# Kernel optimization log

Hardware: AMD Instinct MI355X
Metric: run time of the kernel (lower is better)

The kernel has to match this reference:

```python
import jax, jax.numpy as jnp
import numpy as np
from jax import lax

B, C, T, K, L, G = 4, 256, 2048, 7, 2, 32


def _conv1d(x, w, b, pad=0, groups=1):
    # x: [B,C,T], w: [O, C//groups, kw]
    y = lax.conv_general_dilated(x, w, window_strides=(1,), padding=[(pad, pad)],
                                 dimension_numbers=("NCH", "OIH", "NCH"),
                                 feature_group_count=groups)
    return y + b[None, :, None]


def _conv2d(x, w, b, pad=(0, 0), groups=1):
    # x: [B,C,H,W], w: [O, C//groups, kh, kw]
    y = lax.conv_general_dilated(x, w, window_strides=(1, 1),
                                 padding=[(pad[0], pad[0]), (pad[1], pad[1])],
                                 dimension_numbers=("NCHW", "OIHW", "NCHW"),
                                 feature_group_count=groups)
    return y + b[None, :, None, None]


def _knn_dis(x, k):
    # x: [B,C,T] -> neighbor indices [B,T,k] by (negative) squared euclidean distance
    xx = jnp.sum(x * x, axis=1)                       # [B,T]
    inner = jnp.einsum("bcm,bcn->bmn", x, x)          # [B,T,T]
    pd = -xx[:, :, None] + 2.0 * inner - xx[:, None, :]  # -||x_m - x_n||^2
    _, idx = lax.top_k(pd, k)                          # nearest = largest of -dist^2
    return idx


def _graph_feature(x, idx):
    # x: [B,C,T], idx: [B,T,K] -> style=1 feature [B,2C,T,K] = cat(neighbor, center)
    xt = jnp.transpose(x, (0, 2, 1))                   # [B,T,C]
    bidx = jnp.arange(x.shape[0])[:, None, None]
    nb = xt[bidx, idx]                                 # [B,T,K,C] gather
    ctr = jnp.broadcast_to(xt[:, :, None, :], nb.shape)
    feat = jnp.concatenate([nb, ctr], axis=-1)         # [B,T,K,2C]
    return jnp.transpose(feat, (0, 3, 1, 2))           # [B,2C,T,K]


def setup_inputs() -> dict:
    key = jax.random.key(0)
    ks = jax.random.split(key, 9)
    s = 0.05
    return {
        "x": jax.random.normal(ks[0], (B, C, T), jnp.float32),
        "tw1": jax.random.normal(ks[1], (L, C, C, 1), jnp.float32) * s,
        "tb1": jax.random.normal(ks[2], (L, C), jnp.float32) * s,
        "tw2": jax.random.normal(ks[3], (L, C, C // G, 5), jnp.float32) * s,
        "tb2": jax.random.normal(ks[4], (L, C), jnp.float32) * s,
        "dw1": jax.random.normal(ks[5], (L, C, 2 * C, 1, 1), jnp.float32) * s,
        "db1": jax.random.normal(ks[6], (L, C), jnp.float32) * s,
        "dw2": jax.random.normal(ks[7], (L, C, C // G, 5, 5), jnp.float32) * s,
        "db2": jax.random.normal(ks[8], (L, C), jnp.float32) * s,
    }


def reference(x, tw1, tb1, tw2, tb2, dw1, db1, dw2, db2):
    for i in range(L):
        identity = x
        # temporal branch: 1x1 conv -> GELU -> grouped conv1d k=5 (pad=2)
        h = jax.nn.gelu(_conv1d(x, tw1[i], tb1[i]), approximate=False)
        tout = _conv1d(h, tw2[i], tb2[i], pad=2, groups=G)            # [B,C,T]
        # dynamic graph branch: euclidean knn -> gather -> DConv2D -> max over k
        idx = _knn_dis(x, K)                                           # [B,T,K]
        feat = _graph_feature(x, idx)                                  # [B,2C,T,K]
        g = jax.nn.gelu(_conv2d(feat, dw1[i], db1[i]), approximate=False)
        g = _conv2d(g, dw2[i], db2[i], pad=(2, 2), groups=G)          # [B,C,T,K]
        dout = jnp.max(g, axis=-1)                                     # [B,C,T]
        x = tout + dout + identity
    return x
```

## Files before the change

kernel.cpp:

```cpp
#include <hip/hip_runtime.h>
#include <math.h>

#define Bq 4
#define Cc 256
#define Tt 2048
#define Kk 7
#define NTOP 10
#define CG 8
#define Ll 2
#define NO 768

typedef __attribute__((ext_vector_type(8))) short short8;
typedef __attribute__((ext_vector_type(4))) float floatx4;
typedef __attribute__((ext_vector_type(2))) float floatx2;

__device__ __forceinline__ float gelu_f(float v) {
  return 0.5f * v * (1.0f + erff(v * 0.70710678118654752440f));
}

__device__ __forceinline__ float erf_fast(float x) {
  float ax = fabsf(x);
  float t = __builtin_amdgcn_rcpf(fmaf(0.3275911f, ax, 1.0f));
  float y = t * (0.254829592f + t * (-0.284496736f + t * (1.421413741f +
            t * (-1.453152027f + t * 1.061405429f))));
  float r = 1.0f - y * __expf(-ax * ax);
  return copysignf(r, x);
}
__device__ __forceinline__ float gelu_fast(float v) {
  return 0.5f * v * (1.0f + erf_fast(v * 0.70710678118654752440f));
}

__global__ void transpose_x(const float* __restrict__ x, float* __restrict__ xT,
                            unsigned short* __restrict__ xh,
                            unsigned short* __restrict__ xl) {
  __shared__ float tile[32][33];
  int b = blockIdx.z;
  int t0 = blockIdx.x * 32, c0 = blockIdx.y * 32;
  int tx = threadIdx.x, ty = threadIdx.y;
  const float* xb = x + (size_t)b * Cc * Tt;
  for (int r = ty; r < 32; r += 8)
    tile[r][tx] = xb[(size_t)(c0 + r) * Tt + t0 + tx];
  __syncthreads();
  size_t base = (size_t)b * Tt * Cc;
  for (int r = ty; r < 32; r += 8) {
    float v = tile[tx][r];
    size_t o = base + (size_t)(t0 + r) * Cc + c0 + tx;
    xT[o] = v;
    unsigned int u = __float_as_uint(v);
    unsigned short h = (unsigned short)((u + 0x7fffu + ((u >> 16) & 1u)) >> 16);
    float f = v - __uint_as_float((unsigned int)h << 16);
    unsigned int ul = __float_as_uint(f);
    xh[o] = h;
    xl[o] = (unsigned short)((ul + 0x7fffu + ((ul >> 16) & 1u)) >> 16);
  }
}

__global__ __launch_bounds__(512) void sqnorm_xt(
    const float* __restrict__ xT, float* __restrict__ xx) {
  int b = blockIdx.y;
  int t = blockIdx.x * 8 + (threadIdx.x >> 6);
  int lane = threadIdx.x & 63;
  const float* row = xT + ((size_t)b * Tt + t) * Cc;
  float4 v = *(const float4*)(row + lane * 4);
  float acc = v.x * v.x + v.y * v.y + v.z * v.z + v.w * v.w;
#pragma unroll
  for (int off = 1; off < 64; off <<= 1) acc += __shfl_xor(acc, off);
  if (lane == 0) xx[(size_t)b * Tt + t] = acc;
}

__global__ __launch_bounds__(256) void pw_conv8_all(
    const float* __restrict__ x, const float* __restrict__ tw1,
    const float* __restrict__ tb1, const float* __restrict__ dw1,
    const float* __restrict__ db1, float* __restrict__ hb,
    float* __restrict__ cb, float* __restrict__ nt) {
  int tid = threadIdx.x;
  int wv = tid >> 6, lane = tid & 63;
  int t = blockIdx.x * 1024 + wv * 256 + lane * 4;
  int oy = blockIdx.y;
  int b = blockIdx.z;
  int range = oy >> 5;
  int o0 = (oy & 31) * 8;
  const float* W; int wstride, woff; const float* bias; int dg;
  if (range == 0)      { W = tw1; wstride = Cc;     woff = 0;  bias = tb1;     dg = 1; }
  else if (range == 1) { W = dw1; wstride = 2 * Cc; woff = Cc; bias = db1;     dg = 0; }
  else                 { W = dw1; wstride = 2 * Cc; woff = 0;  bias = nullptr; dg = 0; }
  const float* xp = x + (size_t)b * Cc * Tt + t;
  const float* wp = W + (size_t)o0 * wstride + woff;
  float acc[8][4];
#pragma unroll
  for (int j = 0; j < 8; ++j) {
    float bv = bias ? bias[o0 + j] : 0.f;
#pragma unroll
    for (int e = 0; e < 4; ++e) acc[j][e] = bv;
  }
  for (int c = 0; c < Cc; c += 4) {
    float4 xv0 = *(const float4*)(xp + (size_t)c * Tt);
    float4 xv1 = *(const float4*)(xp + (size_t)(c + 1) * Tt);
    float4 xv2 = *(const float4*)(xp + (size_t)(c + 2) * Tt);
    float4 xv3 = *(const float4*)(xp + (size_t)(c + 3) * Tt);
    float x0[4] = {xv0.x, xv0.y, xv0.z, xv0.w};
    float x1[4] = {xv1.x, xv1.y, xv1.z, xv1.w};
    float x2[4] = {xv2.x, xv2.y, xv2.z, xv2.w};
    float x3[4] = {xv3.x, xv3.y, xv3.z, xv3.w};
#pragma unroll
    for (int j = 0; j < 8; ++j) {
      const float* wr = wp + (size_t)j * wstride + c;
      float w0 = wr[0], w1 = wr[1], w2 = wr[2], w3 = wr[3];
#pragma unroll
      for (int e = 0; e < 4; ++e) {
        float a = acc[j][e];
        a = fmaf(w0, x0[e], a);
        a = fmaf(w1, x1[e], a);
        a = fmaf(w2, x2[e], a);
        a = fmaf(w3, x3[e], a);
        acc[j][e] = a;
      }
    }
  }
  if (range == 2) {
    float* nb0 = nt + ((size_t)b * Tt + t) * Cc + o0;
#pragma unroll
    for (int e = 0; e < 4; ++e) {
      float4 r0, r1;
      r0.x = acc[0][e]; r0.y = acc[1][e]; r0.z = acc[2][e]; r0.w = acc[3][e];
      r1.x = acc[4][e]; r1.y = acc[5][e]; r1.z = acc[6][e]; r1.w = acc[7][e];
      *(float4*)&nb0[(size_t)e * Cc] = r0;
      *(float4*)&nb0[(size_t)e * Cc + 4] = r1;
    }
  } else {
    float* dst = (range == 0) ? hb : cb;
#pragma unroll
    for (int j = 0; j < 8; ++j) {
      float4 r;
      float* rp = (float*)&r;
#pragma unroll
      for (int e = 0; e < 4; ++e) {
        float v = acc[j][e];
        if (dg) v = gelu_f(v);
        rp[e] = v;
      }
      *(float4*)&dst[((size_t)b * Cc + o0 + j) * Tt + t] = r;
    }
  }
}

__global__ __launch_bounds__(256) void wsplit(
    const float* __restrict__ tw1, const float* __restrict__ dw1,
    unsigned short* __restrict__ wh, unsigned short* __restrict__ wl) {
  int o = blockIdx.x;
  int c = threadIdx.x;
  float v;
  if (o < 256) v = tw1[(size_t)o * Cc + c];
  else if (o < 512) v = dw1[(size_t)(o - 256) * (2 * Cc) + Cc + c];
  else v = dw1[(size_t)(o - 512) * (2 * Cc) + c];
  unsigned int u = __float_as_uint(v);
  unsigned short h = (unsigned short)((u + 0x7fffu + ((u >> 16) & 1u)) >> 16);
  float f = v - __uint_as_float((unsigned int)h << 16);
  unsigned int ul = __float_as_uint(f);
  wh[(size_t)o * Cc + c] = h;
  wl[(size_t)o * Cc + c] = (unsigned short)((ul + 0x7fffu + ((ul >> 16) & 1u)) >> 16);
}

__global__ __launch_bounds__(256) void pw_gemm(
    const unsigned short* __restrict__ wh, const unsigned short* __restrict__ wl,
    const unsigned short* __restrict__ xh, const unsigned short* __restrict__ xl,
    const float* __restrict__ tb1, const float* __restrict__ db1,
    float* __restrict__ hb, float* __restrict__ cb, float* __restrict__ nt) {
  __shared__ __align__(16) unsigned short Ah[128][40], Al[128][40];
  __shared__ __align__(16) unsigned short Bh[128][40], Bl[128][40];
  int mt = blockIdx.x;
  int b = mt >> 4;
  int t0 = (mt & 15) * 128;
  int o0 = blockIdx.y * 128;
  int tid = threadIdx.x;
  int w = tid >> 6, lane = tid & 63, quad = lane >> 4, l15 = lane & 15;
  int wm = (w >> 1) * 64, wn = (w & 1) * 64;
  floatx4 acc[4][4];
#pragma unroll
  for (int i = 0; i < 4; ++i)
#pragma unroll
    for (int j = 0; j < 4; ++j) acc[i][j] = (floatx4){0.f, 0.f, 0.f, 0.f};

  const unsigned short* xhb = xh + ((size_t)b * Tt + t0) * Cc;
  const unsigned short* xlb = xl + ((size_t)b * Tt + t0) * Cc;
  int sr = tid >> 1;
  int sq = (tid & 1) * 2;
  for (int kc = 0; kc < Cc; kc += 32) {
    __syncthreads();
    {
      const unsigned short* am = wh + (size_t)(o0 + sr) * Cc + kc + sq * 8;
      *(uint4*)&Ah[sr][sq * 8] = *(const uint4*)am;
      *(uint4*)&Ah[sr][sq * 8 + 8] = *(const uint4*)(am + 8);
      const unsigned short* al = wl + (size_t)(o0 + sr) * Cc + kc + sq * 8;
      *(uint4*)&Al[sr][sq * 8] = *(const uint4*)al;
      *(uint4*)&Al[sr][sq * 8 + 8] = *(const uint4*)(al + 8);
      const unsigned short* bm = xhb + (size_t)sr * Cc + kc + sq * 8;
      *(uint4*)&Bh[sr][sq * 8] = *(const uint4*)bm;
      *(uint4*)&Bh[sr][sq * 8 + 8] = *(const uint4*)(bm + 8);
      const unsigned short* bl = xlb + (size_t)sr * Cc + kc + sq * 8;
      *(uint4*)&Bl[sr][sq * 8] = *(const uint4*)bl;
      *(uint4*)&Bl[sr][sq * 8 + 8] = *(const uint4*)(bl + 8);
    }
    __syncthreads();
    int ka = quad * 8;
    short8 a_h[4], a_l[4], b_h[4], b_l[4];
#pragma unroll
    for (int f = 0; f < 4; ++f) {
      a_h[f] = *(const short8*)&Ah[wm + f * 16 + l15][ka];
      a_l[f] = *(const short8*)&Al[wm + f * 16 + l15][ka];
      b_h[f] = *(const short8*)&Bh[wn + f * 16 + l15][ka];
      b_l[f] = *(const short8*)&Bl[wn + f * 16 + l15][ka];
    }
#pragma unroll
    for (int fm = 0; fm < 4; ++fm)
#pragma unroll
      for (int fn = 0; fn < 4; ++fn) {
        acc[fm][fn] = __builtin_amdgcn_mfma_f32_16x16x32_bf16(a_h[fm], b_h[fn], acc[fm][fn], 0, 0, 0);
        acc[fm][fn] = __builtin_amdgcn_mfma_f32_16x16x32_bf16(a_h[fm], b_l[fn], acc[fm][fn], 0, 0, 0);
        acc[fm][fn] = __builtin_amdgcn_mfma_f32_16x16x32_bf16(a_l[fm], b_h[fn], acc[fm][fn], 0, 0, 0);
      }
  }
  int range = o0 >> 8;
  int ol0 = o0 & 255;
  if (range == 2) {
#pragma unroll
    for (int fm = 0; fm < 4; ++fm) {
      int o = ol0 + wm + fm * 16 + quad * 4;
#pragma unroll
      for (int r = 0; r < 4; ++r) {
#pragma unroll
        for (int fn = 0; fn < 4; ++fn) {
          int t = wn + fn * 16 + l15;
          nt[((size_t)b * Tt + t0 + t) * Cc + o + r] = acc[fm][fn][r];
        }
      }
    }
  } else {
    float* dst = (range == 0) ? hb : cb;
    const float* bias = (range == 0) ? tb1 : db1;
#pragma unroll
    for (int fm = 0; fm < 4; ++fm) {
      int o = ol0 + wm + fm * 16 + quad * 4;
#pragma unroll
      for (int r = 0; r < 4; ++r) {
        float bv = bias[o + r];
        size_t rowoff = ((size_t)b * Cc + o + r) * Tt + t0;
#pragma unroll
        for (int fn = 0; fn < 4; ++fn) {
          int t = wn + fn * 16 + l15;
          float v = acc[fm][fn][r] + bv;
          if (range == 0) v = gelu_f(v);
          dst[rowoff + t] = v;
        }
      }
    }
  }
}

__global__ __launch_bounds__(256) void score_gemm(
    const unsigned short* __restrict__ xh, const unsigned short* __restrict__ xl,
    const float* __restrict__ xx, float* __restrict__ S, int bbase) {
  __shared__ __align__(16) unsigned short Ah[128][40], Al[128][40];
  __shared__ __align__(16) unsigned short Bh[128][40], Bl[128][40];
  int lb = blockIdx.z;
  int b = bbase + lb;
  int m0 = blockIdx.y * 128, n0 = blockIdx.x * 128;
  int tid = threadIdx.x;
  int w = tid >> 6, lane = tid & 63, quad = lane >> 4, l15 = lane & 15;
  int wm = (w >> 1) * 64, wn = (w & 1) * 64;
  const unsigned short* xhb = xh + (size_t)b * Tt * Cc;
  const unsigned short* xlb = xl + (size_t)b * Tt * Cc;
  const float* xxb = xx + (size_t)b * Tt;
  float* Sb = S + (size_t)lb * Tt * Tt;
  floatx4 acc[4][4];
#pragma unroll
  for (int i = 0; i < 4; ++i)
#pragma unroll
    for (int j = 0; j < 4; ++j) acc[i][j] = (floatx4){0.f, 0.f, 0.f, 0.f};

  int sr = tid >> 1;
  int sq = (tid & 1) * 2;
  for (int kc = 0; kc < Cc; kc += 32) {
    __syncthreads();
    {
      const unsigned short* am = xhb + (size_t)(m0 + sr) * Cc + kc + sq * 8;
      *(uint4*)&Ah[sr][sq * 8] = *(const uint4*)am;
      *(uint4*)&Ah[sr][sq * 8 + 8] = *(const uint4*)(am + 8);
      const unsigned short* al = xlb + (size_t)(m0 + sr) * Cc + kc + sq * 8;
      *(uint4*)&Al[sr][sq * 8] = *(const uint4*)al;
      *(uint4*)&Al[sr][sq * 8 + 8] = *(const uint4*)(al + 8);
      const unsigned short* bm = xhb + (size_t)(n0 + sr) * Cc + kc + sq * 8;
      *(uint4*)&Bh[sr][sq * 8] = *(const uint4*)bm;
      *(uint4*)&Bh[sr][sq * 8 + 8] = *(const uint4*)(bm + 8);
      const unsigned short* bl = xlb + (size_t)(n0 + sr) * Cc + kc + sq * 8;
      *(uint4*)&Bl[sr][sq * 8] = *(const uint4*)bl;
      *(uint4*)&Bl[sr][sq * 8 + 8] = *(const uint4*)(bl + 8);
    }
    __syncthreads();
    int ka = quad * 8;
    short8 a_h[4], a_l[4], b_h[4], b_l[4];
#pragma unroll
    for (int f = 0; f < 4; ++f) {
      a_h[f] = *(const short8*)&Ah[wm + f * 16 + l15][ka];
      a_l[f] = *(const short8*)&Al[wm + f * 16 + l15][ka];
      b_h[f] = *(const short8*)&Bh[wn + f * 16 + l15][ka];
      b_l[f] = *(const short8*)&Bl[wn + f * 16 + l15][ka];
    }
#pragma unroll
    for (int fm = 0; fm < 4; ++fm)
#pragma unroll
      for (int fn = 0; fn < 4; ++fn) {
        acc[fm][fn] = __builtin_amdgcn_mfma_f32_16x16x32_bf16(a_h[fm], b_h[fn], acc[fm][fn], 0, 0, 0);
        acc[fm][fn] = __builtin_amdgcn_mfma_f32_16x16x32_bf16(a_h[fm], b_l[fn], acc[fm][fn], 0, 0, 0);
        acc[fm][fn] = __builtin_amdgcn_mfma_f32_16x16x32_bf16(a_l[fm], b_h[fn], acc[fm][fn], 0, 0, 0);
      }
  }
#pragma unroll
  for (int fn = 0; fn < 4; ++fn) {
    int n = n0 + wn + fn * 16 + l15;
    float xv = xxb[n];
#pragma unroll
    for (int fm = 0; fm < 4; ++fm) {
      int m = m0 + wm + fm * 16 + quad * 4;
#pragma unroll
      for (int r = 0; r < 4; ++r)
        Sb[(size_t)(m + r) * Tt + n] = fmaf(2.f, acc[fm][fn][r], -xv);
    }
  }
}

__global__ __launch_bounds__(512) void topk_scan(
    const float* __restrict__ S, int* __restrict__ idx10, int bbase) {
  int lb = blockIdx.z;
  int m = blockIdx.x * 8 + (threadIdx.x >> 6);
  int lane = threadIdx.x & 63;
  const float* row = S + ((size_t)lb * Tt + m) * Tt;
  float s[NTOP]; int idl[NTOP];
#pragma unroll
  for (int j = 0; j < NTOP; ++j) { s[j] = -INFINITY; idl[j] = 0x7fffffff; }
  for (int c0 = lane * 4; c0 < Tt; c0 += 256) {
    float4 v = *(const float4*)(row + c0);
    float cand[4] = {v.x, v.y, v.z, v.w};
#pragma unroll
    for (int e = 0; e < 4; ++e) {
      float sc = cand[e];
      if (sc > s[NTOP - 1]) {
        s[NTOP - 1] = sc; idl[NTOP - 1] = c0 + e;
#pragma unroll
        for (int j = NTOP - 1; j > 0; --j) {
          if (s[j] > s[j - 1]) {
            float ts = s[j]; s[j] = s[j - 1]; s[j - 1] = ts;
            int ti = idl[j]; idl[j] = idl[j - 1]; idl[j - 1] = ti;
          }
        }
      }
    }
  }
  int ptr = 0;
  for (int r = 0; r < NTOP; ++r) {
    float cs = (ptr < NTOP) ? s[ptr] : -INFINITY;
    int cid = (ptr < NTOP) ? idl[ptr] : 0x7fffffff;
    float bs = cs; int bi = cid;
#pragma unroll
    for (int off = 1; off < 64; off <<= 1) {
      float os = __shfl_xor(bs, off);
      int oi = __shfl_xor(bi, off);
      if (os > bs || (os == bs && oi < bi)) { bs = os; bi = oi; }
    }
    if (cid == bi) ptr++;
    if (lane == 0) idx10[((size_t)(bbase + lb) * Tt + m) * NTOP + r] = bi;
  }
}

__global__ __launch_bounds__(256) void knn_rescore(
    const float* __restrict__ xT, const int* __restrict__ idx10,
    int* __restrict__ idxout) {
  int t = blockIdx.x * 4 + (threadIdx.x >> 6);
  int b = blockIdx.y;
  int lane = threadIdx.x & 63;
  int cand = lane & 15;
  int part = lane >> 4;
  const float* xTb = xT + (size_t)b * Tt * Cc;
  const float* xm = xTb + (size_t)t * Cc;
  double dot = 0.0, nn = 0.0;
  int j = 0x7fffffff;
  bool act = (cand < NTOP);
  if (act) {
    j = idx10[((size_t)b * Tt + t) * NTOP + cand];
    const float* xn = xTb + (size_t)j * Cc;
    int c0 = part * 64;
    for (int c = c0; c < c0 + 64; c += 4) {
      float4 a = *(const float4*)(xm + c);
      float4 v = *(const float4*)(xn + c);
      dot += (double)a.x * v.x + (double)a.y * v.y + (double)a.z * v.z + (double)a.w * v.w;
      nn  += (double)v.x * v.x + (double)v.y * v.y + (double)v.z * v.z + (double)v.w * v.w;
    }
  }
  dot += __shfl_xor(dot, 16);
  nn  += __shfl_xor(nn, 16);
  dot += __shfl_xor(dot, 32);
  nn  += __shfl_xor(nn, 32);
  double sc = act ? (2.0 * dot - nn) : -1e300;
  int cid = act ? j : 0x7fffffff;
  for (int r = 0; r < Kk; ++r) {
    double bs = sc; int bi = cid;
#pragma unroll
    for (int off = 1; off < 64; off <<= 1) {
      double os = __shfl_xor(bs, off);
      int oi = __shfl_xor(bi, off);
      if (os > bs || (os == bs && oi < bi)) { bs = os; bi = oi; }
    }
    if (cid == bi) { sc = -1e300; cid = 0x7fffffff; }
    if (lane == 0) idxout[((size_t)b * Tt + t) * Kk + r] = bi;
  }
}

template <int FAST>
__global__ __launch_bounds__(256) void graph_tail(
    const float* __restrict__ h, const float* __restrict__ ctr,
    const float* __restrict__ nbrT, const int* __restrict__ idx,
    const float* __restrict__ tw2, const float* __restrict__ tb2,
    const float* __restrict__ dw2, const float* __restrict__ db2,
    const float* __restrict__ xin, float* __restrict__ xout) {
  __shared__ __align__(16) float gt[CG][Kk][68];
  __shared__ __align__(16) float ht[CG][68];
  __shared__ __align__(16) float ct[CG][68];
  __shared__ int jt[Kk * 68];
  int t0 = blockIdx.x * 64;
  int g = blockIdx.y;
  int b = blockIdx.z;
  int tid = threadIdx.x;
  const float* hg   = h   + ((size_t)b * Cc + g * CG) * Tt;
  const float* ctrg = ctr + ((size_t)b * Cc + g * CG) * Tt;
  const float* nbT  = nbrT + (size_t)b * Tt * Cc + g * CG;

  {
    const int* ib = idx + ((size_t)b * Tt + t0 - 2) * Kk;
    for (int p = tid; p < Kk * 68; p += 256) {
      int k = p / 68, tl = p - k * 68;
      int tg = t0 - 2 + tl;
      jt[p] = (tg >= 0 && tg < Tt) ? ib[tl * Kk + k] : 0;
    }
    for (int e = tid; e < CG * 68; e += 256) {
      int ci = e / 68, tl = e - ci * 68;
      int tg = t0 - 2 + tl;
      int valid = (tg >= 0 && tg < Tt);
      ht[ci][tl] = valid ? hg[(size_t)ci * Tt + tg] : 0.f;
      ct[ci][tl] = valid ? ctrg[(size_t)ci * Tt + tg] : 0.f;
    }
  }
  __syncthreads();
  for (int p = tid; p < Kk * 68; p += 256) {
    int k = p / 68, tl = p - k * 68;
    int tg = t0 - 2 + tl;
    int valid = (tg >= 0 && tg < Tt);
    int j = jt[p];
    const float* np = nbT + (size_t)j * Cc;
    float4 n0 = *(const float4*)np;
    float4 n1 = *(const float4*)(np + 4);
    float ch[8] = {n0.x, n0.y, n0.z, n0.w, n1.x, n1.y, n1.z, n1.w};
#pragma unroll
    for (int ci = 0; ci < CG; ++ci) {
      float pre = ct[ci][tl] + ch[ci];
      float v = FAST ? gelu_fast(pre) : gelu_f(pre);
      gt[ci][k][tl] = valid ? v : 0.f;
    }
  }
  __syncthreads();

  int ol = tid >> 5, tl2 = (tid & 31) * 2;
  int o = g * CG + ol;

  const float* w2 = tw2 + (size_t)o * CG * 5;
  float bt = tb2[o];
  floatx2 acct = {bt, bt};
  for (int ci = 0; ci < CG; ++ci) {
    floatx2 p0 = *(const floatx2*)&ht[ci][tl2];
    floatx2 p1 = *(const floatx2*)&ht[ci][tl2 + 2];
    floatx2 p2 = *(const floatx2*)&ht[ci][tl2 + 4];
    float r6[6] = {p0.x, p0.y, p1.x, p1.y, p2.x, p2.y};
#pragma unroll
    for (int dt = 0; dt < 5; ++dt) {
      float wv = w2[ci * 5 + dt];
      floatx2 wv2 = {wv, wv};
      floatx2 rp = {r6[dt], r6[dt + 1]};
      acct = __builtin_elementwise_fma(wv2, rp, acct);
    }
  }

  const float* wp = dw2 + (size_t)o * CG * 25;
  float bv = db2[o];
  floatx2 acc[Kk];
#pragma unroll
  for (int k = 0; k < Kk; ++k) acc[k] = (floatx2){bv, bv};

  for (int ci = 0; ci < CG; ++ci) {
    float w[25];
#pragma unroll
    for (int i = 0; i < 25; ++i) w[i] = wp[ci * 25 + i];
#pragma unroll
    for (int kin = 0; kin < Kk; ++kin) {
      floatx2 p0 = *(const floatx2*)&gt[ci][kin][tl2];
      floatx2 p1 = *(const floatx2*)&gt[ci][kin][tl2 + 2];
      floatx2 p2 = *(const floatx2*)&gt[ci][kin][tl2 + 4];
      float r6[6] = {p0.x, p0.y, p1.x, p1.y, p2.x, p2.y};
      floatx2 rp[5];
#pragma unroll
      for (int dt = 0; dt < 5; ++dt) rp[dt] = (floatx2){r6[dt], r6[dt + 1]};
#pragma unroll
      for (int dk = 0; dk < 5; ++dk) {
        int k = kin + 2 - dk;
        if (k < 0 || k >= Kk) continue;
#pragma unroll
        for (int dt = 0; dt < 5; ++dt) {
          float wv = w[dt * 5 + dk];
          floatx2 wv2 = {wv, wv};
          acc[k] = __builtin_elementwise_fma(wv2, rp[dt], acc[k]);
        }
      }
    }
  }
  floatx2 m = acc[0];
#pragma unroll
  for (int k = 1; k < Kk; ++k) m = __builtin_elementwise_max(m, acc[k]);
  size_t off = ((size_t)b * Cc + o) * Tt + t0 + tl2;
  floatx2 xv = *(const floatx2*)&xin[off];
  floatx2 r;
  r.x = acct.x + m.x + xv.x;
  r.y = acct.y + m.y + xv.y;
  *(floatx2*)&xout[off] = r;
}

extern "C" void kernel_launch(void* const* d_in, const int* in_sizes, int n_in,
                              void* d_out, int out_size, void* d_ws, size_t ws_size,
                              hipStream_t stream) {
  const float* x0  = (const float*)d_in[0];
  const float* tw1 = (const float*)d_in[1];
  const float* tb1 = (const float*)d_in[2];
  const float* tw2 = (const float*)d_in[3];
  const float* tb2 = (const float*)d_in[4];
  const float* dw1 = (const float*)d_in[5];
  const float* db1 = (const float*)d_in[6];
  const float* dw2 = (const float*)d_in[7];
  const float* db2 = (const float*)d_in[8];
  float* out = (float*)d_out;

  float* ws = (float*)d_ws;
  const size_t NCT = (size_t)Bq * Cc * Tt;
  float* x1   = ws;
  float* hbuf = x1 + NCT;
  float* cbuf = hbuf + NCT;
  float* xT   = cbuf + NCT;
  unsigned short* xh = (unsigned short*)(xT + NCT);
  unsigned short* xl = xh + NCT;
  unsigned short* wh = xl + NCT;
  unsigned short* wl = wh + (size_t)NO * Cc;
  float* S    = (float*)(wl + (size_t)NO * Cc);
  float* xx   = S + 2 * (size_t)Tt * Tt;
  int* idxb   = (int*)(xx + (size_t)Bq * Tt);
  int* idx10  = idxb + (size_t)Bq * Tt * Kk;
  float* nbrT = (float*)(idx10 + (size_t)Bq * Tt * NTOP);

  for (int i = 0; i < Ll; ++i) {
    const float* xin = (i == 0) ? x0 : x1;
    float* xout = (i == Ll - 1) ? out : x1;

    transpose_x<<<dim3(Tt/32, Cc/32, Bq), dim3(32, 8), 0, stream>>>(xin, xT, xh, xl);
    sqnorm_xt<<<dim3(Tt/8, Bq), 512, 0, stream>>>(xT, xx);
    for (int bp = 0; bp < Bq; bp += 2) {
      score_gemm<<<dim3(16, 16, 2), 256, 0, stream>>>(xh, xl, xx, S, bp);
      topk_scan<<<dim3(Tt/8, 1, 2), 512, 0, stream>>>(S, idx10, bp);
    }
    knn_rescore<<<dim3(Tt/4, Bq), 256, 0, stream>>>(xT, idx10, idxb);

    if (i == 0) {
      pw_conv8_all<<<dim3(Tt/1024, 96, Bq), 256, 0, stream>>>(
          xin, tw1 + (size_t)i * Cc * Cc, tb1 + (size_t)i * Cc,
          dw1 + (size_t)i * Cc * 2 * Cc, db1 + (size_t)i * Cc,
          hbuf, cbuf, nbrT);
    } else {
      wsplit<<<dim3(NO), 256, 0, stream>>>(
          tw1 + (size_t)i * Cc * Cc, dw1 + (size_t)i * Cc * 2 * Cc, wh, wl);
      pw_gemm<<<dim3(64, NO/128), 256, 0, stream>>>(
          wh, wl, xh, xl, tb1 + (size_t)i * Cc, db1 + (size_t)i * Cc,
          hbuf, cbuf, nbrT);
    }
    if (i == 0) {
      graph_tail<0><<<dim3(Tt/64, Cc/CG, Bq), 256, 0, stream>>>(
          hbuf, cbuf, nbrT, idxb, tw2 + (size_t)i * Cc * CG * 5, tb2 + (size_t)i * Cc,
          dw2 + (size_t)i * Cc * CG * 25, db2 + (size_t)i * Cc, xin, xout);
    } else {
      graph_tail<1><<<dim3(Tt/64, Cc/CG, Bq), 256, 0, stream>>>(
          hbuf, cbuf, nbrT, idxb, tw2 + (size_t)i * Cc * CG * 5, tb2 + (size_t)i * Cc,
          dw2 + (size_t)i * Cc * CG * 25, db2 + (size_t)i * Cc, xin, xout);
    }
  }
}
```

Before: 525.7 us.

## Fuse score GEMM with per-tile top-k and merge partial candidates in rescore

The score GEMM no longer writes the full TxT distance matrix to global memory. Each 128x128 tile is staged in shared memory and reduced there to a per-row top-10 candidate list, one list per column tile. A new merge kernel combines the 16 partial lists, then does the double-precision rescore in the same kernel. This removes the large score-matrix write and re-read and one kernel launch per batch pair, at the cost of serial wave-level selection loops inside the GEMM kernel and a smaller partial-candidate buffer.

```diff
diff --git a/kernel.cpp b/kernel.cpp
--- a/kernel.cpp
+++ b/kernel.cpp
@@ -9,6 +9,7 @@
 #define CG 8
 #define Ll 2
 #define NO 768
+#define NTILE 16
 
 typedef __attribute__((ext_vector_type(8))) short short8;
 typedef __attribute__((ext_vector_type(4))) float floatx4;
@@ -257,21 +258,28 @@
   }
 }
 
-__global__ __launch_bounds__(256) void score_gemm(
+__global__ __launch_bounds__(256) void score_topk(
     const unsigned short* __restrict__ xh, const unsigned short* __restrict__ xl,
-    const float* __restrict__ xx, float* __restrict__ S, int bbase) {
-  __shared__ __align__(16) unsigned short Ah[128][40], Al[128][40];
-  __shared__ __align__(16) unsigned short Bh[128][40], Bl[128][40];
+    const float* __restrict__ xx, float* __restrict__ Pv, int* __restrict__ Pi,
+    int bbase) {
+  __shared__ __align__(16) char smem[40960];
+  typedef unsigned short ush;
+  ush (*Ah)[40] = (ush(*)[40])smem;
+  ush (*Al)[40] = (ush(*)[40])(smem + 10240);
+  ush (*Bh)[40] = (ush(*)[40])(smem + 20480);
+  ush (*Bl)[40] = (ush(*)[40])(smem + 30720);
+  float (*sst)[132] = (float(*)[132])smem;
+
   int lb = blockIdx.z;
   int b = bbase + lb;
   int m0 = blockIdx.y * 128, n0 = blockIdx.x * 128;
+  int tile = blockIdx.x;
   int tid = threadIdx.x;
   int w = tid >> 6, lane = tid & 63, quad = lane >> 4, l15 = lane & 15;
   int wm = (w >> 1) * 64, wn = (w & 1) * 64;
   const unsigned short* xhb = xh + (size_t)b * Tt * Cc;
   const unsigned short* xlb = xl + (size_t)b * Tt * Cc;
   const float* xxb = xx + (size_t)b * Tt;
-  float* Sb = S + (size_t)lb * Tt * Tt;
   floatx4 acc[4][4];
 #pragma unroll
   for (int i = 0; i < 4; ++i)
@@ -315,51 +323,74 @@
         acc[fm][fn] = __builtin_amdgcn_mfma_f32_16x16x32_bf16(a_l[fm], b_h[fn], acc[fm][fn], 0, 0, 0);
       }
   }
-#pragma unroll
-  for (int fn = 0; fn < 4; ++fn) {
-    int n = n0 + wn + fn * 16 + l15;
-    float xv = xxb[n];
-#pragma unroll
-    for (int fm = 0; fm < 4; ++fm) {
-      int m = m0 + wm + fm * 16 + quad * 4;
-#pragma unroll
-      for (int r = 0; r < 4; ++r)
-        Sb[(size_t)(m + r) * Tt + n] = fmaf(2.f, acc[fm][fn][r], -xv);
-    }
-  }
-}
-
-__global__ __launch_bounds__(512) void topk_scan(
-    const float* __restrict__ S, int* __restrict__ idx10, int bbase) {
-  int lb = blockIdx.z;
-  int m = blockIdx.x * 8 + (threadIdx.x >> 6);
+  __syncthreads();
+
+  for (int half = 0; half < 2; ++half) {
+    if ((w >> 1) == half) {
+#pragma unroll
+      for (int fn = 0; fn < 4; ++fn) {
+        float xv = xxb[n0 + wn + fn * 16 + l15];
+#pragma unroll
+        for (int fm = 0; fm < 4; ++fm)
+#pragma unroll
+          for (int r = 0; r < 4; ++r)
+            sst[fm * 16 + quad * 4 + r][wn + fn * 16 + l15] =
+                fmaf(2.f, acc[fm][fn][r], -xv);
+      }
+    }
+    __syncthreads();
+#pragma unroll 1
+    for (int rr = 0; rr < 16; ++rr) {
+      int row = w * 16 + rr;
+      int m = m0 + half * 64 + row;
+      float v0 = sst[row][lane];
+      float v1 = sst[row][lane + 64];
+      int i0 = n0 + lane, i1 = n0 + lane + 64;
+      if (v1 > v0) { float tv = v0; v0 = v1; v1 = tv; int ti = i0; i0 = i1; i1 = ti; }
+      int ptr = 0;
+      for (int sel = 0; sel < NTOP; ++sel) {
+        float cs = (ptr == 0) ? v0 : (ptr == 1) ? v1 : -INFINITY;
+        int cid = (ptr == 0) ? i0 : (ptr == 1) ? i1 : 0x7fffffff;
+        float bs = cs; int bi = cid;
+#pragma unroll
+        for (int off = 1; off < 64; off <<= 1) {
+          float os = __shfl_xor(bs, off);
+          int oi = __shfl_xor(bi, off);
+          if (os > bs || (os == bs && oi < bi)) { bs = os; bi = oi; }
+        }
+        if (cid == bi) ptr++;
+        if (lane == 0) {
+          size_t po = ((size_t)b * Tt + m) * (NTILE * NTOP) + (size_t)tile * NTOP + sel;
+          Pv[po] = bs;
+          Pi[po] = bi;
+        }
+      }
+    }
+    __syncthreads();
+  }
+}
+
+__global__ __launch_bounds__(512) void merge_rescore(
+    const float* __restrict__ Pv, const int* __restrict__ Pi,
+    const float* __restrict__ xT, int* __restrict__ idxout) {
+  __shared__ int cl[8][16];
+  int b = blockIdx.y;
+  int wv = threadIdx.x >> 6;
+  int m = blockIdx.x * 8 + wv;
   int lane = threadIdx.x & 63;
-  const float* row = S + ((size_t)lb * Tt + m) * Tt;
-  float s[NTOP]; int idl[NTOP];
-#pragma unroll
-  for (int j = 0; j < NTOP; ++j) { s[j] = -INFINITY; idl[j] = 0x7fffffff; }
-  for (int c0 = lane * 4; c0 < Tt; c0 += 256) {
-    float4 v = *(const float4*)(row + c0);
-    float cand[4] = {v.x, v.y, v.z, v.w};
-#pragma unroll
-    for (int e = 0; e < 4; ++e) {
-      float sc = cand[e];
-      if (sc > s[NTOP - 1]) {
-        s[NTOP - 1] = sc; idl[NTOP - 1] = c0 + e;
-#pragma unroll
-        for (int j = NTOP - 1; j > 0; --j) {
-          if (s[j] > s[j - 1]) {
-            float ts = s[j]; s[j] = s[j - 1]; s[j - 1] = ts;
-            int ti = idl[j]; idl[j] = idl[j - 1]; idl[j - 1] = ti;
-          }
-        }
-      }
-    }
-  }
+  const float* pv = Pv + ((size_t)b * Tt + m) * (NTILE * NTOP);
+  const int*   pi = Pi + ((size_t)b * Tt + m) * (NTILE * NTOP);
+  float v0 = pv[lane], v1 = pv[lane + 64];
+  int   i0 = pi[lane], i1 = pi[lane + 64];
+  float v2 = -INFINITY; int i2 = 0x7fffffff;
+  if (lane < 32) { v2 = pv[lane + 128]; i2 = pi[lane + 128]; }
+  if (v1 > v0 || (v1 == v0 && i1 < i0)) { float t = v0; v0 = v1; v1 = t; int u = i0; i0 = i1; i1 = u; }
+  if (v2 > v1 || (v2 == v1 && i2 < i1)) { float t = v1; v1 = v2; v2 = t; int u = i1; i1 = i2; i2 = u; }
+  if (v1 > v0 || (v1 == v0 && i1 < i0)) { float t = v0; v0 = v1; v1 = t; int u = i0; i0 = i1; i1 = u; }
   int ptr = 0;
   for (int r = 0; r < NTOP; ++r) {
-    float cs = (ptr < NTOP) ? s[ptr] : -INFINITY;
-    int cid = (ptr < NTOP) ? idl[ptr] : 0x7fffffff;
+    float cs = (ptr == 0) ? v0 : (ptr == 1) ? v1 : (ptr == 2) ? v2 : -INFINITY;
+    int cid = (ptr == 0) ? i0 : (ptr == 1) ? i1 : (ptr == 2) ? i2 : 0x7fffffff;
     float bs = cs; int bi = cid;
 #pragma unroll
     for (int off = 1; off < 64; off <<= 1) {
@@ -368,25 +399,17 @@
       if (os > bs || (os == bs && oi < bi)) { bs = os; bi = oi; }
     }
     if (cid == bi) ptr++;
-    if (lane == 0) idx10[((size_t)(bbase + lb) * Tt + m) * NTOP + r] = bi;
-  }
-}
-
-__global__ __launch_bounds__(256) void knn_rescore(
-    const float* __restrict__ xT, const int* __restrict__ idx10,
-    int* __restrict__ idxout) {
-  int t = blockIdx.x * 4 + (threadIdx.x >> 6);
-  int b = blockIdx.y;
-  int lane = threadIdx.x & 63;
-  int cand = lane & 15;
-  int part = lane >> 4;
+    if (lane == 0) cl[wv][r] = bi;
+  }
+  __syncthreads();
+  int cand = lane & 15, part = lane >> 4;
   const float* xTb = xT + (size_t)b * Tt * Cc;
-  const float* xm = xTb + (size_t)t * Cc;
+  const float* xm = xTb + (size_t)m * Cc;
   double dot = 0.0, nn = 0.0;
   int j = 0x7fffffff;
   bool act = (cand < NTOP);
   if (act) {
-    j = idx10[((size_t)b * Tt + t) * NTOP + cand];
+    j = cl[wv][cand];
     const float* xn = xTb + (size_t)j * Cc;
     int c0 = part * 64;
     for (int c = c0; c < c0 + 64; c += 4) {
@@ -411,7 +434,7 @@
       if (os > bs || (os == bs && oi < bi)) { bs = os; bi = oi; }
     }
     if (cid == bi) { sc = -1e300; cid = 0x7fffffff; }
-    if (lane == 0) idxout[((size_t)b * Tt + t) * Kk + r] = bi;
+    if (lane == 0) idxout[((size_t)b * Tt + m) * Kk + r] = bi;
   }
 }
 
@@ -555,11 +578,11 @@
   unsigned short* xl = xh + NCT;
   unsigned short* wh = xl + NCT;
   unsigned short* wl = wh + (size_t)NO * Cc;
-  float* S    = (float*)(wl + (size_t)NO * Cc);
-  float* xx   = S + 2 * (size_t)Tt * Tt;
+  float* Pv   = (float*)(wl + (size_t)NO * Cc);
+  int*   Pi   = (int*)(Pv + (size_t)Bq * Tt * NTILE * NTOP);
+  float* xx   = (float*)(Pi + (size_t)Bq * Tt * NTILE * NTOP);
   int* idxb   = (int*)(xx + (size_t)Bq * Tt);
-  int* idx10  = idxb + (size_t)Bq * Tt * Kk;
-  float* nbrT = (float*)(idx10 + (size_t)Bq * Tt * NTOP);
+  float* nbrT = (float*)(idxb + (size_t)Bq * Tt * Kk);
 
   for (int i = 0; i < Ll; ++i) {
     const float* xin = (i == 0) ? x0 : x1;
@@ -568,10 +591,9 @@
     transpose_x<<<dim3(Tt/32, Cc/32, Bq), dim3(32, 8), 0, stream>>>(xin, xT, xh, xl);
     sqnorm_xt<<<dim3(Tt/8, Bq), 512, 0, stream>>>(xT, xx);
     for (int bp = 0; bp < Bq; bp += 2) {
-      score_gemm<<<dim3(16, 16, 2), 256, 0, stream>>>(xh, xl, xx, S, bp);
-      topk_scan<<<dim3(Tt/8, 1, 2), 512, 0, stream>>>(S, idx10, bp);
-    }
-    knn_rescore<<<dim3(Tt/4, Bq), 256, 0, stream>>>(xT, idx10, idxb);
+      score_topk<<<dim3(NTILE, 16, 2), 256, 0, stream>>>(xh, xl, xx, Pv, Pi, bp);
+    }
+    merge_rescore<<<dim3(Tt/8, Bq), 512, 0, stream>>>(Pv, Pi, xT, idxb);
 
     if (i == 0) {
       pw_conv8_all<<<dim3(Tt/1024, 96, Bq), 256, 0, stream>>>(
```

New measurement: 1.162 ms. 121% more time.
